# Kernel tuning notes

Hardware: AMD Instinct MI355X
Metric: run time of the kernel (lower is better)

The kernel has to match this reference:

```python
import jax, jax.numpy as jnp
import numpy as np

D_MODEL = 768
N_HEADS = 12
HEAD_DIM = D_MODEL // N_HEADS
NEG = -10000.0


def setup_inputs() -> dict:
    key = jax.random.key(0)
    ks = jax.random.split(key, 8)
    B, S, D = 2, 2048, D_MODEL
    inp = {
        "q": jax.random.normal(ks[0], (B, S, D), dtype=jnp.float32),
        "k": jax.random.normal(ks[1], (B, S, D), dtype=jnp.float32),
        "v": jax.random.normal(ks[2], (B, S, D), dtype=jnp.float32),
        "attn_mask": jax.random.randint(ks[3], (B, S), 0, 2, dtype=jnp.int32),
        # weights stored [in, out]; apply as x @ W (equivalent to torch Linear)
        "Wq": jax.random.normal(ks[4], (D, D), dtype=jnp.float32) / np.sqrt(D),
        "Wk": jax.random.normal(ks[5], (D, D), dtype=jnp.float32) / np.sqrt(D),
        "Wv": jax.random.normal(ks[6], (D, D), dtype=jnp.float32) / np.sqrt(D),
        "Wo": jax.random.normal(ks[7], (D, D), dtype=jnp.float32) / np.sqrt(D),
        "mask_future": 1,
    }
    return inp


def reference(q, k, v, attn_mask, Wq, Wk, Wv, Wo, mask_future):
    B, S, D = q.shape
    H, hd = N_HEADS, HEAD_DIM
    # project and split heads -> [B, H, S, hd]
    qh = (q @ Wq).reshape(B, S, H, hd).transpose(0, 2, 1, 3)
    kh = (k @ Wk).reshape(B, S, H, hd).transpose(0, 2, 1, 3)
    vh = (v @ Wv).reshape(B, S, H, hd).transpose(0, 2, 1, 3)

    scale = 1.0 / np.sqrt(hd).astype(np.float32)
    # full [B, H, L, S] score matrix (naive SDPA, as in the original)
    scores = jnp.einsum("bhld,bhsd->bhls", qh, kh) * scale
    if mask_future:
        causal = jnp.triu(jnp.full((S, S), NEG, dtype=scores.dtype), k=1)
        scores = scores + causal
    # padding mask: [B, S] -> broadcast over heads and query positions
    pad = attn_mask[:, None, None, :] == 0
    scores = jnp.where(pad, NEG, scores)
    attn = jax.nn.softmax(scores, axis=-1)  # dropout p=0.0 -> identity
    out = jnp.einsum("bhls,bhsd->bhld", attn, vh)  # [B, H, L, hd]
    out = out.transpose(0, 2, 1, 3).reshape(B, S, D)
    return out @ Wo
```

## Files before the change

kernel.cpp:

```cpp
#include <hip/hip_runtime.h>


#define NEGV (-10000.0f)

typedef __attribute__((ext_vector_type(8))) short v8s;
typedef __attribute__((ext_vector_type(4))) float v4f;
typedef __attribute__((ext_vector_type(8))) unsigned short v8u;

__device__ __forceinline__ unsigned short f2bf(float f) {
  unsigned int u = __float_as_uint(f);
  u += 0x7FFFu + ((u >> 16) & 1u);
  return (unsigned short)(u >> 16);
}

__global__ __launch_bounds__(256) void transpose_w(
    const float* __restrict__ w0, const float* __restrict__ w1,
    const float* __restrict__ w2, const float* __restrict__ w3,
    unsigned short* __restrict__ t0, unsigned short* __restrict__ t1,
    unsigned short* __restrict__ t2, unsigned short* __restrict__ t3) {
  const float* w; unsigned short* t;
  switch (blockIdx.z) {
    case 0: w = w0; t = t0; break;
    case 1: w = w1; t = t1; break;
    case 2: w = w2; t = t2; break;
    default: w = w3; t = t3; break;
  }
  __shared__ unsigned short tile[32][33];
  const int tx = threadIdx.x & 31, ty = threadIdx.x >> 5;
  const int x0 = blockIdx.x * 32, y0 = blockIdx.y * 32;
#pragma unroll
  for (int j = 0; j < 4; j++)
    tile[ty + j * 8][tx] = f2bf(w[(size_t)(y0 + ty + j * 8) * 768 + x0 + tx]);
  __syncthreads();
#pragma unroll
  for (int j = 0; j < 4; j++)
    t[(size_t)(x0 + ty + j * 8) * 768 + y0 + tx] = tile[tx][ty + j * 8];
}

template <bool ABF16HEAD, bool CF32ROW>
__device__ __forceinline__ void gemm_core(const void* __restrict__ A,
                                          const unsigned short* __restrict__ Wt,
                                          void* __restrict__ C) {
  const int tid = threadIdx.x;
  const int wave = tid >> 6, lane = tid & 63;
  const int quad = lane >> 4, l16 = lane & 15;
  const int wm = wave >> 1, wn = wave & 1;
  const int bm = blockIdx.x * 128, bn = blockIdx.y * 128;

  __shared__ __align__(16) unsigned short As[128 * 32];
  __shared__ __align__(16) unsigned short Bs[128 * 32];

  v4f acc[4][4];
#pragma unroll
  for (int i = 0; i < 4; i++)
#pragma unroll
    for (int j = 0; j < 4; j++) acc[i][j] = (v4f){0.f, 0.f, 0.f, 0.f};

  for (int kt = 0; kt < 24; kt++) {
    __syncthreads();
#pragma unroll
    for (int p = 0; p < 2; p++) {
      int idx = p * 256 + tid;
      int r = idx >> 2, c0 = (idx & 3) << 3;
      int rg = bm + r, c = kt * 32 + c0;
      if (ABF16HEAD) {
        size_t aoff = ((size_t)((rg >> 11) * 12 + (c >> 6)) * 2048 +
                       (rg & 2047)) * 64 + (c & 63);
        *(uint4*)&As[r * 32 + c0] =
            *(const uint4*)((const unsigned short*)A + aoff);
      } else {
        const float* Af = (const float*)A;
        size_t aoff = (size_t)rg * 768 + c;
        float4 x0 = *(const float4*)(Af + aoff);
        float4 x1 = *(const float4*)(Af + aoff + 4);
        v8u tmp;
        tmp[0] = f2bf(x0.x); tmp[1] = f2bf(x0.y);
        tmp[2] = f2bf(x0.z); tmp[3] = f2bf(x0.w);
        tmp[4] = f2bf(x1.x); tmp[5] = f2bf(x1.y);
        tmp[6] = f2bf(x1.z); tmp[7] = f2bf(x1.w);
        *(uint4*)&As[r * 32 + c0] = *(uint4*)&tmp;
      }
      *(uint4*)&Bs[r * 32 + c0] =
          *(const uint4*)&Wt[(size_t)(bn + r) * 768 + c];
    }
    __syncthreads();

    v8s aF[4], bF[4];
#pragma unroll
    for (int mt = 0; mt < 4; mt++)
      aF[mt] = *(const v8s*)&As[(wm * 64 + mt * 16 + l16) * 32 + quad * 8];
#pragma unroll
    for (int nt = 0; nt < 4; nt++)
      bF[nt] = *(const v8s*)&Bs[(wn * 64 + nt * 16 + l16) * 32 + quad * 8];
#pragma unroll
    for (int mt = 0; mt < 4; mt++)
#pragma unroll
      for (int nt = 0; nt < 4; nt++)
        acc[mt][nt] = __builtin_amdgcn_mfma_f32_16x16x32_bf16(
            aF[mt], bF[nt], acc[mt][nt], 0, 0, 0);
  }

#pragma unroll
  for (int mt = 0; mt < 4; mt++) {
#pragma unroll
    for (int i = 0; i < 4; i++) {
      int row = bm + wm * 64 + mt * 16 + quad * 4 + i;
#pragma unroll
      for (int nt = 0; nt < 4; nt++) {
        int col = bn + wn * 64 + nt * 16 + l16;
        if (CF32ROW) {
          ((float*)C)[(size_t)row * 768 + col] = acc[mt][nt][i];
        } else {
          size_t off = ((size_t)((row >> 11) * 12 + (col >> 6)) * 2048 +
                        (row & 2047)) * 64 + (col & 63);
          ((unsigned short*)C)[off] = f2bf(acc[mt][nt][i]);
        }
      }
    }
  }
}

__global__ __launch_bounds__(256) void gemm_qkv(
    const float* __restrict__ xq, const float* __restrict__ xk,
    const float* __restrict__ xv, const unsigned short* __restrict__ wqt,
    const unsigned short* __restrict__ wkt, const unsigned short* __restrict__ wvt,
    unsigned short* __restrict__ qh, unsigned short* __restrict__ kh,
    unsigned short* __restrict__ vh) {
  const float* A; const unsigned short* Wt; unsigned short* C;
  switch (blockIdx.z) {
    case 0: A = xq; Wt = wqt; C = qh; break;
    case 1: A = xk; Wt = wkt; C = kh; break;
    default: A = xv; Wt = wvt; C = vh; break;
  }
  gemm_core<false, false>((const void*)A, Wt, (void*)C);
}

__global__ __launch_bounds__(256) void gemm_o(
    const unsigned short* __restrict__ oat, const unsigned short* __restrict__ wot,
    float* __restrict__ out) {
  gemm_core<true, true>((const void*)oat, wot, (void*)out);
}

__global__ __launch_bounds__(256) void attn_kernel(
    const unsigned short* __restrict__ qh, const unsigned short* __restrict__ kh,
    const unsigned short* __restrict__ vh, const int* __restrict__ attn_mask,
    const int* __restrict__ mask_future, unsigned short* __restrict__ o) {
  const int S = 2048, HD = 64, NH = 12;
  const int qt = blockIdx.x;
  const int bh = blockIdx.y;
  const int b = bh / NH, h = bh % NH;
  const int tid = threadIdx.x;
  const int wave = tid >> 6, lane = tid & 63;
  const int quad = lane >> 4, l16 = lane & 15;

  __shared__ __align__(16) unsigned short Ks[64 * 72];
  __shared__ __align__(16) unsigned short Vt[64 * 72];
  __shared__ __align__(16) unsigned short Ps[4][16 * 72];
  __shared__ int Ms[64];
  __shared__ int s_flag;

  const size_t head_off = (size_t)(b * NH + h) * S * HD;
  const unsigned short* Kb = kh + head_off;
  const unsigned short* Vb = vh + head_off;

  const int mf = mask_future[0];
  if (tid == 0) s_flag = 0;

  const int qrowA = qt * 64 + wave * 16 + l16;
  v8s aQ[2];
  {
    const unsigned short* qp = qh + head_off + (size_t)qrowA * HD + quad * 8;
    aQ[0] = *(const v8s*)(qp);
    aQ[1] = *(const v8s*)(qp + 32);
  }
  const int qbase = qt * 64 + wave * 16 + quad * 4;

  float m_i[4], l_i[4];
  v4f accO[4];
#pragma unroll
  for (int i = 0; i < 4; i++) { m_i[i] = -1e30f; l_i[i] = 0.f; }
#pragma unroll
  for (int dt = 0; dt < 4; dt++) accO[dt] = (v4f){0.f, 0.f, 0.f, 0.f};

  const int kt_causal = mf ? qt : (S / 64 - 1);

  for (int phase = 0; phase < 2; phase++) {
    int kt_lo, kt_hi;
    if (phase == 0) { kt_lo = 0; kt_hi = kt_causal; }
    else {
      bool need = (m_i[0] < -5000.f) || (m_i[1] < -5000.f) ||
                  (m_i[2] < -5000.f) || (m_i[3] < -5000.f);
      if (need) s_flag = 1;
      __syncthreads();
      if (!s_flag) break;
      kt_lo = kt_causal + 1; kt_hi = S / 64 - 1;
    }
    for (int kt = kt_lo; kt <= kt_hi; kt++) {
      __syncthreads();
      {
        const uint4* srck = (const uint4*)(Kb + (size_t)kt * 64 * HD);
        const uint4* srcv = (const uint4*)(Vb + (size_t)kt * 64 * HD);
#pragma unroll
        for (int p = 0; p < 2; p++) {
          int idx = p * 256 + tid;
          int r = idx >> 3;
          int c0 = (idx & 7) << 3;
          *(uint4*)&Ks[r * 72 + c0] = srck[idx];
          v8u vv;
          *(uint4*)&vv = srcv[idx];
          int shift = (idx & 7) << 3;
#pragma unroll
          for (int i = 0; i < 8; i++) {
            int d = c0 + i;
            int scol = (r + shift) & 63;
            Vt[d * 72 + scol] = vv[i];
          }
        }
        if (tid < 64) Ms[tid] = attn_mask[b * S + kt * 64 + tid];
      }
      __syncthreads();

      v4f sc[4];
#pragma unroll
      for (int nt = 0; nt < 4; nt++) {
        const unsigned short* kp = &Ks[(nt * 16 + l16) * 72 + quad * 8];
        v8s b0 = *(const v8s*)kp;
        v8s b1 = *(const v8s*)(kp + 32);
        v4f z = (v4f){0.f, 0.f, 0.f, 0.f};
        z = __builtin_amdgcn_mfma_f32_16x16x32_bf16(aQ[0], b0, z, 0, 0, 0);
        z = __builtin_amdgcn_mfma_f32_16x16x32_bf16(aQ[1], b1, z, 0, 0, 0);
        sc[nt] = z;
      }

#pragma unroll
      for (int nt = 0; nt < 4; nt++) {
        int key = kt * 64 + nt * 16 + l16;
        bool pad = (Ms[nt * 16 + l16] == 0);
#pragma unroll
        for (int i = 0; i < 4; i++) {
          float v = sc[nt][i] * 0.125f;
          v += (mf && (key > qbase + i)) ? NEGV : 0.f;
          v = pad ? NEGV : v;
          sc[nt][i] = v;
        }
      }

#pragma unroll
      for (int i = 0; i < 4; i++) {
        float mx = fmaxf(fmaxf(sc[0][i], sc[1][i]), fmaxf(sc[2][i], sc[3][i]));
        mx = fmaxf(mx, __shfl_xor(mx, 1));
        mx = fmaxf(mx, __shfl_xor(mx, 2));
        mx = fmaxf(mx, __shfl_xor(mx, 4));
        mx = fmaxf(mx, __shfl_xor(mx, 8));
        float mnew = fmaxf(m_i[i], mx);
        float alpha = __expf(m_i[i] - mnew);
        m_i[i] = mnew;
        float rs = 0.f;
#pragma unroll
        for (int nt = 0; nt < 4; nt++) {
          float p = __expf(sc[nt][i] - mnew);
          sc[nt][i] = p;
          rs += p;
        }
        rs += __shfl_xor(rs, 1);
        rs += __shfl_xor(rs, 2);
        rs += __shfl_xor(rs, 4);
        rs += __shfl_xor(rs, 8);
        l_i[i] = l_i[i] * alpha + rs;
#pragma unroll
        for (int dt = 0; dt < 4; dt++) accO[dt][i] *= alpha;
      }

#pragma unroll
      for (int nt = 0; nt < 4; nt++)
#pragma unroll
        for (int i = 0; i < 4; i++)
          Ps[wave][(quad * 4 + i) * 72 + nt * 16 + l16] = f2bf(sc[nt][i]);

#pragma unroll
      for (int ks = 0; ks < 2; ks++) {
        v8s aP = *(const v8s*)&Ps[wave][l16 * 72 + ks * 32 + quad * 8];
#pragma unroll
        for (int dt = 0; dt < 4; dt++) {
          int d = dt * 16 + l16;
          int scol = ((ks * 32 + quad * 8) + ((d >> 3) << 3)) & 63;
          v8s bV = *(const v8s*)&Vt[d * 72 + scol];
          accO[dt] =
              __builtin_amdgcn_mfma_f32_16x16x32_bf16(aP, bV, accO[dt], 0, 0, 0);
        }
      }
    }
    if (phase == 0) __syncthreads();
  }

#pragma unroll
  for (int i = 0; i < 4; i++) {
    float inv = 1.f / l_i[i];
    int qr = qbase + i;
    size_t base = head_off + (size_t)qr * HD;
#pragma unroll
    for (int dt = 0; dt < 4; dt++)
      o[base + dt * 16 + l16] = f2bf(accO[dt][i] * inv);
  }
}

extern "C" void kernel_launch(void* const* d_in, const int* in_sizes, int n_in,
                              void* d_out, int out_size, void* d_ws, size_t ws_size,
                              hipStream_t stream) {
  const float* q  = (const float*)d_in[0];
  const float* k  = (const float*)d_in[1];
  const float* v  = (const float*)d_in[2];
  const int* amask = (const int*)d_in[3];
  const float* Wq = (const float*)d_in[4];
  const float* Wk = (const float*)d_in[5];
  const float* Wv = (const float*)d_in[6];
  const float* Wo = (const float*)d_in[7];
  const int* mf  = (const int*)d_in[8];
  float* out = (float*)d_out;

  unsigned short* ws = (unsigned short*)d_ws;
  unsigned short* qh = ws;
  unsigned short* kh = qh + 3145728;
  unsigned short* vh = kh + 3145728;
  unsigned short* wqt = vh + 3145728;
  unsigned short* wkt = wqt + 589824;
  unsigned short* wvt = wkt + 589824;
  unsigned short* wot = wvt + 589824;

  transpose_w<<<dim3(24, 24, 4), 256, 0, stream>>>(Wq, Wk, Wv, Wo,
                                                   wqt, wkt, wvt, wot);
  gemm_qkv<<<dim3(32, 6, 3), 256, 0, stream>>>(q, k, v, wqt, wkt, wvt,
                                               qh, kh, vh);
  attn_kernel<<<dim3(32, 24), 256, 0, stream>>>(qh, kh, vh, amask, mf, qh);
  gemm_o<<<dim3(32, 6), 256, 0, stream>>>(qh, wot, out);
}
```

Measured before the change: 249.7 us.

## Prefetch next K/V tile into registers, reorder causal blocks, raise MFMA priority

```diff
diff --git a/kernel.cpp b/kernel.cpp
--- a/kernel.cpp
+++ b/kernel.cpp
@@ -146,9 +146,14 @@
     const unsigned short* __restrict__ vh, const int* __restrict__ attn_mask,
     const int* __restrict__ mask_future, unsigned short* __restrict__ o) {
   const int S = 2048, HD = 64, NH = 12;
-  const int qt = blockIdx.x;
-  const int bh = blockIdx.y;
+
+  const int nlin = blockIdx.x + 32 * blockIdx.y;
+  const int m_ = nlin & 255, t_ = nlin >> 8;
+  const int i_ = (t_ == 1) ? (511 - m_) : (t_ * 256 + m_);
+  const int qt = 31 - i_ / 24;
+  const int bh = i_ - (i_ / 24) * 24;
   const int b = bh / NH, h = bh % NH;
+
   const int tid = threadIdx.x;
   const int wave = tid >> 6, lane = tid & 63;
   const int quad = lane >> 4, l16 = lane & 15;
@@ -183,6 +188,39 @@
   for (int dt = 0; dt < 4; dt++) accO[dt] = (v4f){0.f, 0.f, 0.f, 0.f};
 
   const int kt_causal = mf ? qt : (S / 64 - 1);
+
+  uint4 pk0, pk1, pv0, pv1;
+  int pm = 0;
+  bool have = false;
+
+  auto prefetch = [&](int kt) {
+    const uint4* srck = (const uint4*)(Kb + (size_t)kt * 64 * HD);
+    const uint4* srcv = (const uint4*)(Vb + (size_t)kt * 64 * HD);
+    pk0 = srck[tid];
+    pk1 = srck[256 + tid];
+    pv0 = srcv[tid];
+    pv1 = srcv[256 + tid];
+    if (tid < 64) pm = attn_mask[b * S + kt * 64 + tid];
+  };
+
+  auto stage = [&]() {
+#pragma unroll
+    for (int p = 0; p < 2; p++) {
+      int idx = p * 256 + tid;
+      int r = idx >> 3;
+      int c0 = (idx & 7) << 3;
+      *(uint4*)&Ks[r * 72 + c0] = p ? pk1 : pk0;
+      v8u vv;
+      *(uint4*)&vv = p ? pv1 : pv0;
+#pragma unroll
+      for (int i = 0; i < 8; i++) {
+        int d = c0 + i;
+        int scol = (r + c0) & 63;
+        Vt[d * 72 + scol] = vv[i];
+      }
+    }
+    if (tid < 64) Ms[tid] = pm;
+  };
 
   for (int phase = 0; phase < 2; phase++) {
     int kt_lo, kt_hi;
@@ -196,31 +234,22 @@
       kt_lo = kt_causal + 1; kt_hi = S / 64 - 1;
     }
     for (int kt = kt_lo; kt <= kt_hi; kt++) {
+      if (!have) prefetch(kt);
       __syncthreads();
+      stage();
+      __syncthreads();
+
       {
-        const uint4* srck = (const uint4*)(Kb + (size_t)kt * 64 * HD);
-        const uint4* srcv = (const uint4*)(Vb + (size_t)kt * 64 * HD);
-#pragma unroll
-        for (int p = 0; p < 2; p++) {
-          int idx = p * 256 + tid;
-          int r = idx >> 3;
-          int c0 = (idx & 7) << 3;
-          *(uint4*)&Ks[r * 72 + c0] = srck[idx];
-          v8u vv;
-          *(uint4*)&vv = srcv[idx];
-          int shift = (idx & 7) << 3;
-#pragma unroll
-          for (int i = 0; i < 8; i++) {
-            int d = c0 + i;
-            int scol = (r + shift) & 63;
-            Vt[d * 72 + scol] = vv[i];
-          }
-        }
-        if (tid < 64) Ms[tid] = attn_mask[b * S + kt * 64 + tid];
-      }
-      __syncthreads();
+        int ktn = -1;
+        if (kt < kt_hi) ktn = kt + 1;
+        else if (phase == 0 && mf && kt_causal < S / 64 - 1)
+          ktn = kt_causal + 1;
+        if (ktn >= 0) { prefetch(ktn); have = true; }
+        else have = false;
+      }
 
       v4f sc[4];
+      __builtin_amdgcn_s_setprio(1);
 #pragma unroll
       for (int nt = 0; nt < 4; nt++) {
         const unsigned short* kp = &Ks[(nt * 16 + l16) * 72 + quad * 8];
@@ -231,6 +260,7 @@
         z = __builtin_amdgcn_mfma_f32_16x16x32_bf16(aQ[1], b1, z, 0, 0, 0);
         sc[nt] = z;
       }
+      __builtin_amdgcn_s_setprio(0);
 
 #pragma unroll
       for (int nt = 0; nt < 4; nt++) {
@@ -277,6 +307,7 @@
         for (int i = 0; i < 4; i++)
           Ps[wave][(quad * 4 + i) * 72 + nt * 16 + l16] = f2bf(sc[nt][i]);
 
+      __builtin_amdgcn_s_setprio(1);
 #pragma unroll
       for (int ks = 0; ks < 2; ks++) {
         v8s aP = *(const v8s*)&Ps[wave][l16 * 72 + ks * 32 + quad * 8];
@@ -289,6 +320,7 @@
               __builtin_amdgcn_mfma_f32_16x16x32_bf16(aP, bV, accO[dt], 0, 0, 0);
         }
       }
+      __builtin_amdgcn_s_setprio(0);
     }
     if (phase == 0) __syncthreads();
   }
```

Result: faster. 234.4 us (-6.1%).
